# Kernel tuning notes

Measured on AMD Instinct MI355X. Metric: run time of the kernel, lower is better.

Reference implementation:

```python
import jax, jax.numpy as jnp
import numpy as np

EPS = 1e-6
NUM_HEADS = 16

def _feature_map(x):
    # elu(x) + 1
    return jnp.where(x > 0, x + 1.0, jnp.exp(x))

def setup_inputs() -> dict:
    key = jax.random.key(0)
    ks = jax.random.split(key, 7)
    B, L, S, D = 4, 4096, 4096, 2048
    sc = 1.0 / np.sqrt(D)
    return {
        "query": jax.random.normal(ks[0], (B, L, D), jnp.float32),
        "kv": jax.random.normal(ks[1], (B, S, D), jnp.float32),
        "Wq": jax.random.normal(ks[2], (D, D), jnp.float32) * sc,
        "Wg": jax.random.normal(ks[3], (D, D), jnp.float32) * sc,
        "bg": jnp.ones((D,), jnp.float32),
        "Wkv": jax.random.normal(ks[4], (2 * D, D), jnp.float32) * sc,
        "Wo": jax.random.normal(ks[5], (D, D), jnp.float32) * sc,
    }

def reference(query, kv, Wq, Wg, bg, Wkv, Wo):
    B, L, D = query.shape
    S = kv.shape[1]
    H = NUM_HEADS
    hd = D // H
    q = query @ Wq.T                      # [B,L,D]
    gate = jax.nn.sigmoid(query @ Wg.T + bg)  # [B,L,D]
    kvp = kv @ Wkv.T                      # [B,S,2D]
    k, v = jnp.split(kvp, 2, axis=-1)
    # reshape to heads: [B,H,L,hd]
    q = _feature_map(q.reshape(B, L, H, hd).transpose(0, 2, 1, 3))
    k = _feature_map(k.reshape(B, S, H, hd).transpose(0, 2, 1, 3))
    v = v.reshape(B, S, H, hd).transpose(0, 2, 1, 3)
    kv_summary = jnp.einsum('bhsd,bhse->bhde', k, v)   # [B,H,hd,hd]
    k_sum = k.sum(axis=-2)                              # [B,H,hd]
    z = 1.0 / (jnp.einsum('bhld,bhd->bhl', q, k_sum)[..., None] + EPS)
    attn = jnp.einsum('bhld,bhde->bhle', q, kv_summary) * z  # [B,H,L,hd]
    attn = attn.transpose(0, 2, 1, 3).reshape(B, L, D)
    out = (attn * gate) @ Wo.T
    return out
```

## Files before the change

### kernel.cpp

```cpp
#include <hip/hip_runtime.h>

typedef __attribute__((ext_vector_type(8))) short bf16x8;
typedef __attribute__((ext_vector_type(4))) float f32x4;
typedef __attribute__((ext_vector_type(4))) unsigned int u32x4;

constexpr int L_ = 4096, S_ = 4096, D_ = 2048, H_ = 16, HD_ = 128;
constexpr int LDSS = 72;

__device__ __forceinline__ unsigned short f2bf(float f) {
    unsigned int u = __builtin_bit_cast(unsigned int, f);
    return (unsigned short)((u + 0x7fffu + ((u >> 16) & 1u)) >> 16);
}
__device__ __forceinline__ float bf2f(unsigned short h) {
    unsigned int u = ((unsigned int)h) << 16;
    return __builtin_bit_cast(float, u);
}
__device__ __forceinline__ unsigned long long pack4(float a, float b, float c, float d) {
    return (unsigned long long)f2bf(a) | ((unsigned long long)f2bf(b) << 16)
         | ((unsigned long long)f2bf(c) << 32) | ((unsigned long long)f2bf(d) << 48);
}
__device__ __forceinline__ float featmap(float x) {
    return x > 0.f ? x + 1.f : __expf(x);
}
__device__ __forceinline__ void gload16(const unsigned short* g, unsigned short* l) {
    __builtin_amdgcn_global_load_lds(
        (const __attribute__((address_space(1))) void*)g,
        (__attribute__((address_space(3))) void*)l, 16, 0, 0);
}

__global__ __launch_bounds__(256) void cvt_bf16(
    const float* __restrict__ in, unsigned short* __restrict__ out, int n8)
{
    const int stride = gridDim.x * 256;
    for (int i = blockIdx.x * 256 + threadIdx.x; i < n8; i += stride) {
        const float4 a = ((const float4*)in)[2 * i];
        const float4 b = ((const float4*)in)[2 * i + 1];
        unsigned long long* o = (unsigned long long*)&out[(size_t)i * 8];
        o[0] = pack4(a.x, a.y, a.z, a.w);
        o[1] = pack4(b.x, b.y, b.z, b.w);
    }
}

template<int MODE, int NBN>
__global__ __launch_bounds__(512, 2) void gemm256(
    const unsigned short* __restrict__ A, const unsigned short* __restrict__ B,
    unsigned short* __restrict__ C1, unsigned short* __restrict__ C2,
    float* __restrict__ Cf, const float* __restrict__ bias)
{
    __shared__ alignas(16) unsigned short lds[65536];
    const int tid = threadIdx.x;
    const int lane = tid & 63, w = tid >> 6;
    const int wr = w >> 2, wc = w & 3;
    const int lr = lane & 15;
    const int lk8 = (lane >> 4) * 8;
    const int rsw = (lr & 7) << 3;
    const int lsub = lane >> 3;
    const int scol = ((lane & 7) ^ lsub) * 8;

    const int wg = blockIdx.x;
    const int xcd = wg & 7, u = wg >> 3;
    const int s = u >> 2, q = u & 3;
    const int sbm = s & 3, sbn = s >> 2;
    const int bm = xcd * 8 + sbm * 2 + (q & 1);
    const int bn = sbn * 2 + (q >> 1);
    const int row0 = bm * 256, bcol = bn * 256;

    const unsigned short* Ap = A + (size_t)row0 * D_;
    const unsigned short* Bp = B + (size_t)bcol * D_;
    const int rA = w * 8 + lsub;
    const int rB = ((w * 8 + lsub) >> 5) * 64 + ((w * 8 + lsub) & 31);

    f32x4 acc[8][4] = {};
    bf16x8 av[2][4], bv[2][4];

#define STA(BUF, HH, KT) do { \
    const unsigned short* g_ = Ap + (size_t)((HH) * 64 + rA) * D_ + (KT) * 64 + scol; \
    unsigned short* l_ = &lds[(BUF) * 16384 + (HH) * 8192 + w * 512]; \
    gload16(g_, l_); gload16(g_ + (size_t)128 * D_, l_ + 4096); } while (0)

#define STB(BUF, HH, KT) do { \
    const unsigned short* g_ = Bp + (size_t)(rB + (HH) * 32) * D_ + (KT) * 64 + scol; \
    unsigned short* l_ = &lds[32768 + (BUF) * 16384 + (HH) * 8192 + w * 512]; \
    gload16(g_, l_); gload16(g_ + (size_t)128 * D_, l_ + 4096); } while (0)

#define RD_A(MQ, BUF) \
    _Pragma("unroll") for (int mi = 0; mi < 4; mi++) \
    _Pragma("unroll") for (int ks = 0; ks < 2; ks++) \
        av[ks][mi] = *(const bf16x8*)&lds[(BUF) * 16384 + (MQ) * 8192 \
            + (mi * 16 + lr + wr * 64) * 64 + ((ks * 32 + lk8) ^ rsw)];

#define RD_B(NQ, BUF) \
    _Pragma("unroll") for (int j = 0; j < 2; j++) \
    _Pragma("unroll") for (int ks = 0; ks < 2; ks++) \
        bv[ks][(NQ) * 2 + j] = *(const bf16x8*)&lds[32768 + (BUF) * 16384 + (NQ) * 8192 \
            + (j * 16 + lr + wc * 32) * 64 + ((ks * 32 + lk8) ^ rsw)];

#define MFMA_Q(MQ, NQ) \
    __builtin_amdgcn_s_setprio(1); \
    _Pragma("unroll") for (int mi = 0; mi < 4; mi++) \
    _Pragma("unroll") for (int j = 0; j < 2; j++) \
    _Pragma("unroll") for (int ks = 0; ks < 2; ks++) \
        acc[(MQ) * 4 + mi][(NQ) * 2 + j] = __builtin_amdgcn_mfma_f32_16x16x32_bf16( \
            av[ks][mi], bv[ks][(NQ) * 2 + j], acc[(MQ) * 4 + mi][(NQ) * 2 + j], 0, 0, 0); \
    __builtin_amdgcn_s_setprio(0);

#define SB0 __builtin_amdgcn_sched_barrier(0)
#define BAR __builtin_amdgcn_s_barrier()
#define VM6 asm volatile("s_waitcnt vmcnt(6)" ::: "memory")
#define VM0 asm volatile("s_waitcnt vmcnt(0)" ::: "memory")

    STA(0, 0, 0); STB(0, 0, 0); STB(0, 1, 0); STA(0, 1, 0);
    STA(1, 0, 1); STB(1, 0, 1); STB(1, 1, 1);
    VM6;
    BAR;
    RD_B(0, 0); RD_B(1, 0);

    constexpr int NT = D_ / 64;
    for (int i = 0; i < NT / 2 - 1; i++) {
        const int T = 2 * i;
        RD_A(0, 0); STA(1, 1, T + 1);
        MFMA_Q(0, 0); SB0; BAR;
        STA(0, 0, T + 2);
        MFMA_Q(0, 1); SB0; BAR;
        RD_A(1, 0); STB(0, 0, T + 2);
        MFMA_Q(1, 1); SB0; BAR;
        STB(0, 1, T + 2);
        MFMA_Q(1, 0);
        VM6; RD_B(0, 1); RD_B(1, 1);
        SB0; BAR;
        RD_A(0, 1); STA(0, 1, T + 2);
        MFMA_Q(0, 0); SB0; BAR;
        STA(1, 0, T + 3);
        MFMA_Q(0, 1); SB0; BAR;
        RD_A(1, 1); STB(1, 0, T + 3);
        MFMA_Q(1, 1); SB0; BAR;
        STB(1, 1, T + 3);
        MFMA_Q(1, 0);
        VM6; RD_B(0, 0); RD_B(1, 0);
        SB0; BAR;
    }
    {
        RD_A(0, 0); STA(1, 1, NT - 1);
        MFMA_Q(0, 0); SB0; BAR;
        MFMA_Q(0, 1); SB0; BAR;
        RD_A(1, 0);
        MFMA_Q(1, 1); SB0; BAR;
        MFMA_Q(1, 0);
        VM0; RD_B(0, 1); RD_B(1, 1);
        SB0; BAR;
        RD_A(0, 1);
        MFMA_Q(0, 0); SB0; BAR;
        MFMA_Q(0, 1); SB0; BAR;
        RD_A(1, 1);
        MFMA_Q(1, 1); SB0; BAR;
        MFMA_Q(1, 0); SB0; BAR;
    }

    const int rb = (lane >> 4) * 4;
    const bool second = bn >= (NBN / 2);
    if (MODE == 1) {
        unsigned short* TT = lds;
        const int b = row0 >> 12;
        #pragma unroll
        for (int qd = 0; qd < 4; qd++) {
            const int sq = qd >> 1, dh = qd & 1;
            __syncthreads();
            if (wr == sq && (wc >> 1) == dh) {
                #pragma unroll
                for (int m = 0; m < 8; m++) {
                    #pragma unroll
                    for (int n = 0; n < 4; n++) {
                        float x0 = acc[m][n][0], x1 = acc[m][n][1];
                        float x2 = acc[m][n][2], x3 = acc[m][n][3];
                        if (!second) {
                            x0 = featmap(x0); x1 = featmap(x1);
                            x2 = featmap(x2); x3 = featmap(x3);
                        }
                        const int dcol = (wc & 1) * 64 + n * 16 + lr;
                        *(unsigned long long*)&TT[dcol * 136 + m * 16 + rb]
                            = pack4(x0, x1, x2, x3);
                    }
                }
            }
            __syncthreads();
            const int h2 = (bn & 7) * 2 + dh;
            const int s0 = (row0 + sq * 128) & (S_ - 1);
            unsigned short* dst = (second ? C2 : C1) + (size_t)(b * H_ + h2) * HD_ * S_;
            #pragma unroll
            for (int it = 0; it < 4; it++) {
                const int idx = it * 512 + tid;
                const int d = idx >> 4, sc2 = (idx & 15) * 8;
                *(u32x4*)&dst[(size_t)d * S_ + s0 + sc2] = *(const u32x4*)&TT[d * 136 + sc2];
            }
        }
        return;
    }
    #pragma unroll
    for (int m = 0; m < 8; m++) {
        #pragma unroll
        for (int n = 0; n < 4; n++) {
            #pragma unroll
            for (int r = 0; r < 4; r++) {
                const size_t gr = (size_t)(row0 + wr * 128 + m * 16 + rb + r);
                const int gc = bcol + wc * 64 + n * 16 + lr;
                float x = acc[m][n][r];
                if (MODE == 0) {
                    if (!second) {
                        C1[gr * D_ + gc] = f2bf(featmap(x));
                    } else {
                        const int gc2 = gc - D_;
                        float t = x + bias[gc2];
                        C2[gr * D_ + gc2] = f2bf(1.f / (1.f + __expf(-t)));
                    }
                } else {
                    Cf[gr * D_ + gc] = x;
                }
            }
        }
    }
#undef STA
#undef STB
#undef RD_A
#undef RD_B
#undef MFMA_Q
#undef SB0
#undef BAR
#undef VM6
#undef VM0
}

__global__ __launch_bounds__(256) void kvsum_part(
    const unsigned short* __restrict__ kT, const unsigned short* __restrict__ vT,
    float* __restrict__ part, float* __restrict__ ksum_part)
{
    __shared__ unsigned short kA[HD_ * LDSS];
    __shared__ unsigned short vB[HD_ * LDSS];
    __shared__ float red[HD_ * 8];
    const int tid = threadIdx.x;
    const int cx = blockIdx.x, bh = blockIdx.y;
    const int lane = tid & 63, w = tid >> 6;
    const int wm = (w >> 1) * 64, wn = (w & 1) * 64;
    const int lr = lane & 15, lk = (lane >> 4) * 8;
    const unsigned short* kb = kT + (size_t)bh * HD_ * S_;
    const unsigned short* vb = vT + (size_t)bh * HD_ * S_;
    f32x4 acc[4][4] = {};
    float ksl[4] = {0.f, 0.f, 0.f, 0.f};
    const int chunk = S_ / 8;
    const int s_begin = cx * chunk;
    for (int s0 = s_begin; s0 < s_begin + chunk; s0 += 64) {
        #pragma unroll
        for (int i = 0; i < 4; i++) {
            int idx = tid + i * 256;
            int d = idx >> 3, sc = (idx & 7) * 8;
            u32x4 kk = *(const u32x4*)&kb[(size_t)d * S_ + s0 + sc];
            *(u32x4*)&kA[d * LDSS + sc] = kk;
            unsigned short t8[8];
            *(u32x4*)t8 = kk;
            float ss = 0.f;
            #pragma unroll
            for (int j = 0; j < 8; j++) ss += bf2f(t8[j]);
            ksl[i] += ss;
            *(u32x4*)&vB[d * LDSS + sc] = *(const u32x4*)&vb[(size_t)d * S_ + s0 + sc];
        }
        __syncthreads();
        #pragma unroll
        for (int ks = 0; ks < 64; ks += 32) {
            bf16x8 av[4], bv[4];
            #pragma unroll
            for (int mi = 0; mi < 4; mi++)
                av[mi] = *(const bf16x8*)&kA[(wm + mi * 16 + lr) * LDSS + ks + lk];
            #pragma unroll
            for (int ni = 0; ni < 4; ni++)
                bv[ni] = *(const bf16x8*)&vB[(wn + ni * 16 + lr) * LDSS + ks + lk];
            #pragma unroll
            for (int mi = 0; mi < 4; mi++)
                #pragma unroll
                for (int ni = 0; ni < 4; ni++)
                    acc[mi][ni] = __builtin_amdgcn_mfma_f32_16x16x32_bf16(
                        av[mi], bv[ni], acc[mi][ni], 0, 0, 0);
        }
        __syncthreads();
    }
    #pragma unroll
    for (int i = 0; i < 4; i++) red[((tid >> 3) + 32 * i) * 8 + (tid & 7)] = ksl[i];
    __syncthreads();
    if (tid < HD_) {
        float s = 0.f;
        #pragma unroll
        for (int j = 0; j < 8; j++) s += red[tid * 8 + j];
        ksum_part[(size_t)cx * (64 * HD_) + bh * HD_ + tid] = s;
    }
    const int rb = (lane >> 4) * 4;
    float* pp = part + ((size_t)cx * 64 + bh) * (HD_ * HD_);
    #pragma unroll
    for (int mi = 0; mi < 4; mi++)
        #pragma unroll
        for (int ni = 0; ni < 4; ni++)
            #pragma unroll
            for (int r = 0; r < 4; r++)
                pp[(wm + mi * 16 + rb + r) * HD_ + wn + ni * 16 + lr] = acc[mi][ni][r];
}

__global__ __launch_bounds__(256) void kvs_reduce(
    const float* __restrict__ part, unsigned short* __restrict__ kvsT,
    const float* __restrict__ ksum_part, float* __restrict__ ksum)
{
    const int idx = blockIdx.x * 256 + threadIdx.x;
    const int e = idx & 127, d2 = (idx >> 7) & 127, bh = idx >> 14;
    float s = 0.f;
    #pragma unroll
    for (int cx = 0; cx < 8; cx++)
        s += part[((size_t)cx * 64 + bh) * 16384 + d2 * 128 + e];
    kvsT[((size_t)bh * 128 + e) * 128 + d2] = f2bf(s);
    if (idx < 64 * 128) {
        float t = 0.f;
        #pragma unroll
        for (int cx = 0; cx < 8; cx++) t += ksum_part[cx * 8192 + idx];
        ksum[idx] = t;
    }
}

__global__ __launch_bounds__(256) void attn_kernel(
    const unsigned short* __restrict__ qf, const unsigned short* __restrict__ kvsT,
    const float* __restrict__ ksum, const unsigned short* __restrict__ gate,
    unsigned short* __restrict__ y)
{
    __shared__ unsigned short qs[128 * 136];
    __shared__ unsigned short bs[128 * LDSS];
    __shared__ float zl[128];
    const int tid = threadIdx.x;
    const int l0 = blockIdx.x * 128;
    const int h = blockIdx.y, b = blockIdx.z;
    const int bh = b * H_ + h;
    const int lane = tid & 63, w = tid >> 6;
    const int wm = (w >> 1) * 64, wn = (w & 1) * 64;
    const int lr = lane & 15, lk = (lane >> 4) * 8;
    const size_t qbase = (size_t)b * L_ * D_ + (size_t)h * HD_;
    #pragma unroll
    for (int i = 0; i < 8; i++) {
        int idx = tid + i * 256;
        int r = idx >> 4, c = (idx & 15) * 8;
        *(u32x4*)&qs[r * 136 + c] = *(const u32x4*)&qf[qbase + (size_t)(l0 + r) * D_ + c];
    }
    __syncthreads();
    if (tid < 128) {
        const float* kp = ksum + bh * HD_;
        float sden = 0.f;
        #pragma unroll 4
        for (int d2 = 0; d2 < HD_; d2++) sden += bf2f(qs[tid * 136 + d2]) * kp[d2];
        zl[tid] = 1.f / (sden + 1e-6f);
    }
    f32x4 acc[4][4] = {};
    for (int kc = 0; kc < 2; kc++) {
        #pragma unroll
        for (int i = 0; i < 4; i++) {
            int idx = tid + i * 256;
            int e = idx >> 3, dc = (idx & 7) * 8;
            *(u32x4*)&bs[e * LDSS + dc] =
                *(const u32x4*)&kvsT[((size_t)bh * 128 + e) * 128 + kc * 64 + dc];
        }
        __syncthreads();
        #pragma unroll
        for (int ks = 0; ks < 64; ks += 32) {
            bf16x8 av[4], bv[4];
            #pragma unroll
            for (int mi = 0; mi < 4; mi++)
                av[mi] = *(const bf16x8*)&qs[(wm + mi * 16 + lr) * 136 + kc * 64 + ks + lk];
            #pragma unroll
            for (int ni = 0; ni < 4; ni++)
                bv[ni] = *(const bf16x8*)&bs[(wn + ni * 16 + lr) * LDSS + ks + lk];
            #pragma unroll
            for (int mi = 0; mi < 4; mi++)
                #pragma unroll
                for (int ni = 0; ni < 4; ni++)
                    acc[mi][ni] = __builtin_amdgcn_mfma_f32_16x16x32_bf16(
                        av[mi], bv[ni], acc[mi][ni], 0, 0, 0);
        }
        __syncthreads();
    }
    const int rb = (lane >> 4) * 4;
    #pragma unroll
    for (int mi = 0; mi < 4; mi++) {
        #pragma unroll
        for (int ni = 0; ni < 4; ni++) {
            #pragma unroll
            for (int r = 0; r < 4; r++) {
                int ll = wm + mi * 16 + rb + r;
                int e = wn + ni * 16 + lr;
                float attn = acc[mi][ni][r] * zl[ll];
                float g = bf2f(gate[qbase + (size_t)(l0 + ll) * D_ + e]);
                y[qbase + (size_t)(l0 + ll) * D_ + e] = f2bf(attn * g);
            }
        }
    }
}

extern "C" void kernel_launch(void* const* d_in, const int* in_sizes, int n_in,
                              void* d_out, int out_size, void* d_ws, size_t ws_size,
                              hipStream_t stream)
{
    (void)in_sizes; (void)n_in; (void)out_size; (void)ws_size;
    const float* query = (const float*)d_in[0];
    const float* kv    = (const float*)d_in[1];
    const float* Wq    = (const float*)d_in[2];
    const float* Wg    = (const float*)d_in[3];
    const float* bg    = (const float*)d_in[4];
    const float* Wkv   = (const float*)d_in[5];
    const float* Wo    = (const float*)d_in[6];
    float* out = (float*)d_out;
    char* ws = (char*)d_ws;

    unsigned short* q_feat = (unsigned short*)(ws);
    unsigned short* gate   = (unsigned short*)(ws + 67108864);
    unsigned short* kTb    = (unsigned short*)(ws + 134217728);
    unsigned short* vTb    = (unsigned short*)(ws + 201326592);
    char* R = ws + 268435456;
    unsigned short* qbf    = (unsigned short*)(R);
    unsigned short* Wqg    = (unsigned short*)(R + 67108864);
    unsigned short* kvbf   = (unsigned short*)(R);
    unsigned short* Wkvb   = (unsigned short*)(R + 67108864);
    float* part            = (float*)(R);
    float* ksum_part       = (float*)(R + 33554432);
    float* ksum            = (float*)(R + 33816576);
    unsigned short* kvsT   = (unsigned short*)(R + 33849344);
    unsigned short* Wob    = (unsigned short*)(R + 83886080);
    unsigned short* ybuf   = kTb;

    dim3 blk(256, 1, 1);
    dim3 blk512(512, 1, 1);
    cvt_bf16<<<dim3(2048), blk, 0, stream>>>(query, qbf, 4194304);
    cvt_bf16<<<dim3(2048), blk, 0, stream>>>(Wq, Wqg, 524288);
    cvt_bf16<<<dim3(2048), blk, 0, stream>>>(Wg, Wqg + 4194304, 524288);
    cvt_bf16<<<dim3(2048), blk, 0, stream>>>(Wo, Wob, 524288);
    gemm256<0, 16><<<dim3(1024), blk512, 0, stream>>>(qbf, Wqg, q_feat, gate, nullptr, bg);
    cvt_bf16<<<dim3(2048), blk, 0, stream>>>(kv, kvbf, 4194304);
    cvt_bf16<<<dim3(2048), blk, 0, stream>>>(Wkv, Wkvb, 1048576);
    gemm256<1, 16><<<dim3(1024), blk512, 0, stream>>>(kvbf, Wkvb, kTb, vTb, nullptr, nullptr);
    kvsum_part<<<dim3(8, 64), blk, 0, stream>>>(kTb, vTb, part, ksum_part);
    kvs_reduce<<<dim3(4096), blk, 0, stream>>>(part, kvsT, ksum_part, ksum);
    attn_kernel<<<dim3(32, 16, 4), blk, 0, stream>>>(q_feat, kvsT, ksum, gate, ybuf);
    gemm256<2, 8><<<dim3(512), blk512, 0, stream>>>(ybuf, Wob, nullptr, nullptr, out, nullptr);
}
```

Measured before the change: 951.0 us.

## Switch GEMM to 32x32x16 MFMA tiles and merge conversion launches

Replaces the 16x16x32 bf16 MFMA fragments in the 256x256 GEMM with 32x32x16 fragments. This changes the LDS read pattern, the accumulator layout and both epilogues. Larger MFMA tiles cut the number of LDS fragment reads per flop and the instruction count. Separately, the six fp32->bf16 conversion launches are merged into two multi-segment kernels to reduce launch overhead. The risk lies in LDS bank conflicts under the new swizzle, register pressure, and whether the epilogue index mapping is correct.

```diff
diff --git a/kernel.cpp b/kernel.cpp
--- a/kernel.cpp
+++ b/kernel.cpp
@@ -2,6 +2,7 @@
 
 typedef __attribute__((ext_vector_type(8))) short bf16x8;
 typedef __attribute__((ext_vector_type(4))) float f32x4;
+typedef __attribute__((ext_vector_type(16))) float f32x16;
 typedef __attribute__((ext_vector_type(4))) unsigned int u32x4;
 
 constexpr int L_ = 4096, S_ = 4096, D_ = 2048, H_ = 16, HD_ = 128;
@@ -28,14 +29,23 @@
         (__attribute__((address_space(3))) void*)l, 16, 0, 0);
 }
 
-__global__ __launch_bounds__(256) void cvt_bf16(
-    const float* __restrict__ in, unsigned short* __restrict__ out, int n8)
-{
+__global__ __launch_bounds__(256) void cvt4(
+    const float* __restrict__ s0, unsigned short* __restrict__ d0, int n0,
+    const float* __restrict__ s1, unsigned short* __restrict__ d1, int n1,
+    const float* __restrict__ s2, unsigned short* __restrict__ d2, int n2,
+    const float* __restrict__ s3, unsigned short* __restrict__ d3, int n3)
+{
+    const int total = n0 + n1 + n2 + n3;
     const int stride = gridDim.x * 256;
-    for (int i = blockIdx.x * 256 + threadIdx.x; i < n8; i += stride) {
-        const float4 a = ((const float4*)in)[2 * i];
-        const float4 b = ((const float4*)in)[2 * i + 1];
-        unsigned long long* o = (unsigned long long*)&out[(size_t)i * 8];
+    for (int i = blockIdx.x * 256 + threadIdx.x; i < total; i += stride) {
+        const float* s; unsigned short* d; int j = i;
+        if (j < n0) { s = s0; d = d0; }
+        else if ((j -= n0) < n1) { s = s1; d = d1; }
+        else if ((j -= n1) < n2) { s = s2; d = d2; }
+        else { j -= n2; s = s3; d = d3; }
+        const float4 a = ((const float4*)s)[2 * (size_t)j];
+        const float4 b = ((const float4*)s)[2 * (size_t)j + 1];
+        unsigned long long* o = (unsigned long long*)&d[(size_t)j * 8];
         o[0] = pack4(a.x, a.y, a.z, a.w);
         o[1] = pack4(b.x, b.y, b.z, b.w);
     }
@@ -51,9 +61,9 @@
     const int tid = threadIdx.x;
     const int lane = tid & 63, w = tid >> 6;
     const int wr = w >> 2, wc = w & 3;
-    const int lr = lane & 15;
-    const int lk8 = (lane >> 4) * 8;
-    const int rsw = (lr & 7) << 3;
+    const int l32 = lane & 31;
+    const int hi = lane >> 5;
+    const int rsw = (lane & 7) << 3;
     const int lsub = lane >> 3;
     const int scol = ((lane & 7) ^ lsub) * 8;
 
@@ -70,8 +80,8 @@
     const int rA = w * 8 + lsub;
     const int rB = ((w * 8 + lsub) >> 5) * 64 + ((w * 8 + lsub) & 31);
 
-    f32x4 acc[8][4] = {};
-    bf16x8 av[2][4], bv[2][4];
+    f32x16 acc[4][2] = {};
+    bf16x8 av[4][2], bv[4][2];
 
 #define STA(BUF, HH, KT) do { \
     const unsigned short* g_ = Ap + (size_t)((HH) * 64 + rA) * D_ + (KT) * 64 + scol; \
@@ -84,24 +94,22 @@
     gload16(g_, l_); gload16(g_ + (size_t)128 * D_, l_ + 4096); } while (0)
 
 #define RD_A(MQ, BUF) \
-    _Pragma("unroll") for (int mi = 0; mi < 4; mi++) \
-    _Pragma("unroll") for (int ks = 0; ks < 2; ks++) \
-        av[ks][mi] = *(const bf16x8*)&lds[(BUF) * 16384 + (MQ) * 8192 \
-            + (mi * 16 + lr + wr * 64) * 64 + ((ks * 32 + lk8) ^ rsw)];
+    _Pragma("unroll") for (int mf = 0; mf < 2; mf++) \
+    _Pragma("unroll") for (int ks = 0; ks < 4; ks++) \
+        av[ks][mf] = *(const bf16x8*)&lds[(BUF) * 16384 + (MQ) * 8192 \
+            + (wr * 64 + mf * 32 + l32) * 64 + ((ks * 16 + hi * 8) ^ rsw)];
 
 #define RD_B(NQ, BUF) \
-    _Pragma("unroll") for (int j = 0; j < 2; j++) \
-    _Pragma("unroll") for (int ks = 0; ks < 2; ks++) \
-        bv[ks][(NQ) * 2 + j] = *(const bf16x8*)&lds[32768 + (BUF) * 16384 + (NQ) * 8192 \
-            + (j * 16 + lr + wc * 32) * 64 + ((ks * 32 + lk8) ^ rsw)];
+    _Pragma("unroll") for (int ks = 0; ks < 4; ks++) \
+        bv[ks][NQ] = *(const bf16x8*)&lds[32768 + (BUF) * 16384 + (NQ) * 8192 \
+            + (wc * 32 + l32) * 64 + ((ks * 16 + hi * 8) ^ rsw)];
 
 #define MFMA_Q(MQ, NQ) \
     __builtin_amdgcn_s_setprio(1); \
-    _Pragma("unroll") for (int mi = 0; mi < 4; mi++) \
-    _Pragma("unroll") for (int j = 0; j < 2; j++) \
-    _Pragma("unroll") for (int ks = 0; ks < 2; ks++) \
-        acc[(MQ) * 4 + mi][(NQ) * 2 + j] = __builtin_amdgcn_mfma_f32_16x16x32_bf16( \
-            av[ks][mi], bv[ks][(NQ) * 2 + j], acc[(MQ) * 4 + mi][(NQ) * 2 + j], 0, 0, 0); \
+    _Pragma("unroll") for (int mf = 0; mf < 2; mf++) \
+    _Pragma("unroll") for (int ks = 0; ks < 4; ks++) \
+        acc[(MQ) * 2 + mf][NQ] = __builtin_amdgcn_mfma_f32_32x32x16_bf16( \
+            av[ks][mf], bv[ks][NQ], acc[(MQ) * 2 + mf][NQ], 0, 0, 0); \
     __builtin_amdgcn_s_setprio(0);
 
 #define SB0 __builtin_amdgcn_sched_barrier(0)
@@ -156,7 +164,6 @@
         MFMA_Q(1, 0); SB0; BAR;
     }
 
-    const int rb = (lane >> 4) * 4;
     const bool second = bn >= (NBN / 2);
     if (MODE == 1) {
         unsigned short* TT = lds;
@@ -167,18 +174,22 @@
             __syncthreads();
             if (wr == sq && (wc >> 1) == dh) {
                 #pragma unroll
-                for (int m = 0; m < 8; m++) {
+                for (int m = 0; m < 4; m++) {
                     #pragma unroll
-                    for (int n = 0; n < 4; n++) {
-                        float x0 = acc[m][n][0], x1 = acc[m][n][1];
-                        float x2 = acc[m][n][2], x3 = acc[m][n][3];
-                        if (!second) {
-                            x0 = featmap(x0); x1 = featmap(x1);
-                            x2 = featmap(x2); x3 = featmap(x3);
+                    for (int nf = 0; nf < 2; nf++) {
+                        #pragma unroll
+                        for (int g = 0; g < 4; g++) {
+                            float x0 = acc[m][nf][4 * g + 0], x1 = acc[m][nf][4 * g + 1];
+                            float x2 = acc[m][nf][4 * g + 2], x3 = acc[m][nf][4 * g + 3];
+                            if (!second) {
+                                x0 = featmap(x0); x1 = featmap(x1);
+                                x2 = featmap(x2); x3 = featmap(x3);
+                            }
+                            const int dcol = (wc & 1) * 64 + nf * 32 + l32;
+                            const int srow = m * 32 + g * 8 + hi * 4;
+                            *(unsigned long long*)&TT[dcol * 136 + srow]
+                                = pack4(x0, x1, x2, x3);
                         }
-                        const int dcol = (wc & 1) * 64 + n * 16 + lr;
-                        *(unsigned long long*)&TT[dcol * 136 + m * 16 + rb]
-                            = pack4(x0, x1, x2, x3);
                     }
                 }
             }
@@ -196,14 +207,15 @@
         return;
     }
     #pragma unroll
-    for (int m = 0; m < 8; m++) {
-        #pragma unroll
-        for (int n = 0; n < 4; n++) {
-            #pragma unroll
-            for (int r = 0; r < 4; r++) {
-                const size_t gr = (size_t)(row0 + wr * 128 + m * 16 + rb + r);
-                const int gc = bcol + wc * 64 + n * 16 + lr;
-                float x = acc[m][n][r];
+    for (int m = 0; m < 4; m++) {
+        #pragma unroll
+        for (int nf = 0; nf < 2; nf++) {
+            #pragma unroll
+            for (int reg = 0; reg < 16; reg++) {
+                const int crow = (reg & 3) + 8 * (reg >> 2) + 4 * hi;
+                const size_t gr = (size_t)(row0 + wr * 128 + m * 32 + crow);
+                const int gc = bcol + wc * 64 + nf * 32 + l32;
+                float x = acc[m][nf][reg];
                 if (MODE == 0) {
                     if (!second) {
                         C1[gr * D_ + gc] = f2bf(featmap(x));
@@ -428,13 +440,15 @@
 
     dim3 blk(256, 1, 1);
     dim3 blk512(512, 1, 1);
-    cvt_bf16<<<dim3(2048), blk, 0, stream>>>(query, qbf, 4194304);
-    cvt_bf16<<<dim3(2048), blk, 0, stream>>>(Wq, Wqg, 524288);
-    cvt_bf16<<<dim3(2048), blk, 0, stream>>>(Wg, Wqg + 4194304, 524288);
-    cvt_bf16<<<dim3(2048), blk, 0, stream>>>(Wo, Wob, 524288);
+    cvt4<<<dim3(2048), blk, 0, stream>>>(query, qbf, 4194304,
+                                         Wq, Wqg, 524288,
+                                         Wg, Wqg + 4194304, 524288,
+                                         Wo, Wob, 524288);
     gemm256<0, 16><<<dim3(1024), blk512, 0, stream>>>(qbf, Wqg, q_feat, gate, nullptr, bg);
-    cvt_bf16<<<dim3(2048), blk, 0, stream>>>(kv, kvbf, 4194304);
-    cvt_bf16<<<dim3(2048), blk, 0, stream>>>(Wkv, Wkvb, 1048576);
+    cvt4<<<dim3(2048), blk, 0, stream>>>(kv, kvbf, 4194304,
+                                         Wkv, Wkvb, 1048576,
+                                         nullptr, nullptr, 0,
+                                         nullptr, nullptr, 0);
     gemm256<1, 16><<<dim3(1024), blk512, 0, stream>>>(kvbf, Wkvb, kTb, vTb, nullptr, nullptr);
     kvsum_part<<<dim3(8, 64), blk, 0, stream>>>(kTb, vTb, part, ksum_part);
     kvs_reduce<<<dim3(4096), blk, 0, stream>>>(part, kvsT, ksum_part, ksum);
```

Result: slower. 1.021 ms (+7.4%).
